# Kernel tuning notes

Measured on AMD Instinct MI355X. Metric: run time of the kernel, lower is better.

The kernel has to match this reference:

```python
import jax, jax.numpy as jnp
import numpy as np

N_CLUSTERS = 128
NUM_ITERS = 10      # fixed Lloyd iterations
LN_EPS = 1e-5       # nn.LayerNorm default eps


def setup_inputs() -> dict:
    key = jax.random.key(0)
    k1, = jax.random.split(key, 1)
    B, N, D = 32, 8192, 64
    patches = jax.random.normal(k1, (B, N, D), dtype=jnp.float32)
    gamma = jnp.ones((D,), dtype=jnp.float32)   # LayerNorm weight
    beta = jnp.zeros((D,), dtype=jnp.float32)   # LayerNorm bias
    return {"patches": patches, "gamma": gamma, "beta": beta}


def _sq_dists(x, x2, c):
    # x: [B,N,D], x2: [B,N,1] (precomputed ||x||^2), c: [B,K,D] -> [B,N,K]
    c2 = jnp.sum(c * c, axis=-1)[:, None, :]                  # [B,1,K]
    return x2 + c2 - 2.0 * jnp.einsum('bnd,bkd->bnk', x, c)


def _kmeans(x):
    B, N, D = x.shape
    K = N_CLUSTERS
    centers0 = x[:, :K, :]                                    # deterministic init: first K points
    x2 = jnp.sum(x * x, axis=-1, keepdims=True)               # [B,N,1]

    def step(c, _):
        d = _sq_dists(x, x2, c)                               # [B,N,K]
        assign = jnp.argmin(d, axis=-1)                       # [B,N]
        oh = jax.nn.one_hot(assign, K, dtype=x.dtype)         # [B,N,K]
        counts = oh.sum(axis=1)                               # [B,K]
        sums = jnp.einsum('bnk,bnd->bkd', oh, x)              # [B,K,D]
        new_c = jnp.where(counts[..., None] > 0,
                          sums / jnp.maximum(counts, 1.0)[..., None],
                          c)                                  # keep empty clusters fixed
        return new_c, None

    centers, _ = jax.lax.scan(step, centers0, None, length=NUM_ITERS)
    dist = _sq_dists(x, x2, centers)                          # [B,N,K]
    soft = jax.nn.softmax(-dist, axis=-1)                     # soft assignment over clusters
    return centers, soft


def reference(patches, gamma, beta):
    # LayerNorm over last dim (biased variance, as in nn.LayerNorm)
    mu = jnp.mean(patches, axis=-1, keepdims=True)
    var = jnp.mean((patches - mu) ** 2, axis=-1, keepdims=True)
    xn = (patches - mu) * jax.lax.rsqrt(var + LN_EPS) * gamma + beta
    centers, soft = _kmeans(xn)
    return centers, soft
```

## Files before the change

### kernel.cpp

```cpp
#include <hip/hip_runtime.h>

#define BATCH 32
#define NPTS  8192
#define DIM   64
#define KC    128
#define NITER 10
#define LN_EPS 1e-5f


__device__ __forceinline__ float dot64(const float4* __restrict__ xv,
                                       const float4* __restrict__ cp) {
    float d0 = 0.f, d1 = 0.f, d2 = 0.f, d3 = 0.f;
#pragma unroll
    for (int j = 0; j < 4; ++j) {
        float4 c0 = cp[4 * j + 0];
        float4 c1 = cp[4 * j + 1];
        float4 c2v = cp[4 * j + 2];
        float4 c3 = cp[4 * j + 3];
        float4 x0 = xv[4 * j + 0];
        float4 x1 = xv[4 * j + 1];
        float4 x2v = xv[4 * j + 2];
        float4 x3 = xv[4 * j + 3];
        d0 = fmaf(x0.w, c0.w, fmaf(x0.z, c0.z, fmaf(x0.y, c0.y, fmaf(x0.x, c0.x, d0))));
        d1 = fmaf(x1.w, c1.w, fmaf(x1.z, c1.z, fmaf(x1.y, c1.y, fmaf(x1.x, c1.x, d1))));
        d2 = fmaf(x2v.w, c2v.w, fmaf(x2v.z, c2v.z, fmaf(x2v.y, c2v.y, fmaf(x2v.x, c2v.x, d2))));
        d3 = fmaf(x3.w, c3.w, fmaf(x3.z, c3.z, fmaf(x3.y, c3.y, fmaf(x3.x, c3.x, d3))));
    }
    return (d0 + d1) + (d2 + d3);
}

__device__ __forceinline__ float sq64(const float4* __restrict__ xv) {
    float a0 = 0.f, a1 = 0.f, a2 = 0.f, a3 = 0.f;
#pragma unroll
    for (int j = 0; j < 16; ++j) {
        float4 t = xv[j];
        a0 = fmaf(t.x, t.x, a0);
        a1 = fmaf(t.y, t.y, a1);
        a2 = fmaf(t.z, t.z, a2);
        a3 = fmaf(t.w, t.w, a3);
    }
    return (a0 + a1) + (a2 + a3);
}

__global__ __launch_bounds__(256) void ln_kernel(const float* __restrict__ patches,
                                                 const float* __restrict__ gamma,
                                                 const float* __restrict__ beta,
                                                 float* __restrict__ xn,
                                                 float* __restrict__ cen,
                                                 float* __restrict__ c2) {
    int row = blockIdx.x * 4 + (threadIdx.x >> 6);
    int lane = threadIdx.x & 63;
    size_t base = (size_t)row * DIM + lane;
    float x = patches[base];

    float s = x;
#pragma unroll
    for (int m = 32; m >= 1; m >>= 1) s += __shfl_xor(s, m, 64);
    float mu = s * (1.0f / 64.0f);
    float dx = x - mu;

    float v = dx * dx;
#pragma unroll
    for (int m = 32; m >= 1; m >>= 1) v += __shfl_xor(v, m, 64);
    float var = v * (1.0f / 64.0f);

    float val = dx * (1.0f / sqrtf(var + LN_EPS)) * gamma[lane] + beta[lane];
    xn[base] = val;

    int n = row & (NPTS - 1);
    int b = row >> 13;
    if (n < KC) {
        cen[((size_t)(b * KC + n)) * DIM + lane] = val;
        float q = val * val;
#pragma unroll
        for (int m = 32; m >= 1; m >>= 1) q += __shfl_xor(q, m, 64);
        if (lane == 0) c2[b * KC + n] = q;
    }
}

__global__ __launch_bounds__(512) void assign_kernel(const float* __restrict__ xn,
                                                     const float* __restrict__ cen,
                                                     const float* __restrict__ c2,
                                                     double* __restrict__ part,
                                                     float* __restrict__ cntpart) {
    __shared__ double ls[KC * 65];
    __shared__ float lc[KC];
    for (int i = threadIdx.x; i < KC * 65; i += 512) ls[i] = 0.0;
    if (threadIdx.x < KC) lc[threadIdx.x] = 0.f;
    __syncthreads();

    int blk = blockIdx.x;
    int b = blk >> 4;
    int p = b * NPTS + ((blk & 15) << 9) + threadIdx.x;

    const float4* xp = (const float4*)(xn + (size_t)p * DIM);
    float4 xv[16];
#pragma unroll
    for (int j = 0; j < 16; ++j) xv[j] = xp[j];
    float x2 = sq64(xv);

    const float4* cp = (const float4*)(cen + (size_t)b * KC * DIM);
    const float* c2p = c2 + b * KC;

    float best = 3.4e38f;
    int bi = 0;
#pragma unroll 2
    for (int k = 0; k < KC; ++k) {
        float dot = dot64(xv, cp + k * 16);
        float t = x2 + c2p[k];
        float d = t - 2.0f * dot;
        if (d < best) { best = d; bi = k; }
    }

    double* dst = ls + bi * 65;
#pragma unroll
    for (int j = 0; j < 16; ++j) {
        atomicAdd(dst + 4 * j + 0, (double)xv[j].x);
        atomicAdd(dst + 4 * j + 1, (double)xv[j].y);
        atomicAdd(dst + 4 * j + 2, (double)xv[j].z);
        atomicAdd(dst + 4 * j + 3, (double)xv[j].w);
    }
    atomicAdd(&lc[bi], 1.0f);
    __syncthreads();

    double* gp = part + (size_t)blk * KC * DIM;
    for (int i = threadIdx.x; i < KC * DIM; i += 512) {
        int k = i >> 6, d = i & 63;
        gp[i] = ls[k * 65 + d];
    }
    if (threadIdx.x < KC) cntpart[blk * KC + threadIdx.x] = lc[threadIdx.x];
}

__global__ __launch_bounds__(256) void update_kernel(const double* __restrict__ part,
                                                     const float* __restrict__ cntpart,
                                                     float* __restrict__ cen,
                                                     float* __restrict__ c2) {
    int row = blockIdx.x * 4 + (threadIdx.x >> 6);
    int lane = threadIdx.x & 63;
    int b = row >> 7;
    int k = row & (KC - 1);

    double s = 0.0;
    float cnt = 0.f;
#pragma unroll
    for (int sub = 0; sub < 16; ++sub) {
        s += part[((size_t)(b * 16 + sub)) * KC * DIM + (size_t)k * DIM + lane];
        cnt += cntpart[(b * 16 + sub) * KC + k];
    }

    size_t idx = (size_t)row * DIM + lane;
    float old = cen[idx];
    float nc = (cnt > 0.f) ? ((float)s / cnt) : old;
    cen[idx] = nc;

    float q = nc * nc;
#pragma unroll
    for (int m = 32; m >= 1; m >>= 1) q += __shfl_xor(q, m, 64);
    if (lane == 0) c2[row] = q;
}

__global__ __launch_bounds__(512) void final_kernel(const float* __restrict__ xn,
                                                    const float* __restrict__ cen,
                                                    const float* __restrict__ c2,
                                                    float* __restrict__ soft) {
    int b = blockIdx.x >> 4;
    int p = b * NPTS + ((blockIdx.x & 15) << 9) + threadIdx.x;

    const float4* xp = (const float4*)(xn + (size_t)p * DIM);
    float4 xv[16];
#pragma unroll
    for (int j = 0; j < 16; ++j) xv[j] = xp[j];
    float x2 = sq64(xv);

    const float4* cp = (const float4*)(cen + (size_t)b * KC * DIM);
    const float* c2p = c2 + b * KC;

    float m = -3.4e38f;
    float ssum = 0.f;
#pragma unroll 2
    for (int k = 0; k < KC; ++k) {
        float dot = dot64(xv, cp + k * 16);
        float t = x2 + c2p[k];
        float z = -(t - 2.0f * dot);
        if (z > m) {
            ssum = ssum * __expf(m - z) + 1.0f;
            m = z;
        } else {
            ssum += __expf(z - m);
        }
    }
    float rinv = 1.0f / ssum;

    float* op = soft + (size_t)p * KC;
#pragma unroll 2
    for (int k = 0; k < KC; ++k) {
        float dot = dot64(xv, cp + k * 16);
        float t = x2 + c2p[k];
        float z = -(t - 2.0f * dot);
        op[k] = __expf(z - m) * rinv;
    }
}

extern "C" void kernel_launch(void* const* d_in, const int* in_sizes, int n_in,
                              void* d_out, int out_size, void* d_ws, size_t ws_size,
                              hipStream_t stream) {
    (void)in_sizes; (void)n_in; (void)out_size; (void)ws_size;
    const float* patches = (const float*)d_in[0];
    const float* gamma = (const float*)d_in[1];
    const float* beta = (const float*)d_in[2];
    float* out = (float*)d_out;

    float* ws = (float*)d_ws;
    float* xn = ws;
    float* cen = xn + (size_t)BATCH * NPTS * DIM;
    float* c2 = cen + (size_t)BATCH * KC * DIM;

    float* soft = out + (size_t)BATCH * KC * DIM;
    double* part = (double*)soft;
    float* cntpart = (float*)(part + (size_t)512 * KC * DIM);

    ln_kernel<<<BATCH * NPTS / 4, 256, 0, stream>>>(patches, gamma, beta, xn, cen, c2);

    for (int it = 0; it < NITER; ++it) {
        assign_kernel<<<BATCH * 16, 512, 0, stream>>>(xn, cen, c2, part, cntpart);
        update_kernel<<<BATCH * KC / 4, 256, 0, stream>>>(part, cntpart, cen, c2);
    }

    hipMemcpyAsync(out, cen, (size_t)BATCH * KC * DIM * sizeof(float),
                   hipMemcpyDeviceToDevice, stream);
    final_kernel<<<BATCH * 16, 512, 0, stream>>>(xn, cen, c2, soft);
}
```

Measured before the change: 1.900 ms.

## Use float LDS atomics, explicit register unrolling, vector soft stores, drop center copy

```diff
diff --git a/kernel.cpp b/kernel.cpp
--- a/kernel.cpp
+++ b/kernel.cpp
@@ -8,39 +8,36 @@
 #define LN_EPS 1e-5f
 
 
-__device__ __forceinline__ float dot64(const float4* __restrict__ xv,
-                                       const float4* __restrict__ cp) {
-    float d0 = 0.f, d1 = 0.f, d2 = 0.f, d3 = 0.f;
-#pragma unroll
-    for (int j = 0; j < 4; ++j) {
-        float4 c0 = cp[4 * j + 0];
-        float4 c1 = cp[4 * j + 1];
-        float4 c2v = cp[4 * j + 2];
-        float4 c3 = cp[4 * j + 3];
-        float4 x0 = xv[4 * j + 0];
-        float4 x1 = xv[4 * j + 1];
-        float4 x2v = xv[4 * j + 2];
-        float4 x3 = xv[4 * j + 3];
-        d0 = fmaf(x0.w, c0.w, fmaf(x0.z, c0.z, fmaf(x0.y, c0.y, fmaf(x0.x, c0.x, d0))));
-        d1 = fmaf(x1.w, c1.w, fmaf(x1.z, c1.z, fmaf(x1.y, c1.y, fmaf(x1.x, c1.x, d1))));
-        d2 = fmaf(x2v.w, c2v.w, fmaf(x2v.z, c2v.z, fmaf(x2v.y, c2v.y, fmaf(x2v.x, c2v.x, d2))));
-        d3 = fmaf(x3.w, c3.w, fmaf(x3.z, c3.z, fmaf(x3.y, c3.y, fmaf(x3.x, c3.x, d3))));
-    }
-    return (d0 + d1) + (d2 + d3);
-}
-
-__device__ __forceinline__ float sq64(const float4* __restrict__ xv) {
-    float a0 = 0.f, a1 = 0.f, a2 = 0.f, a3 = 0.f;
-#pragma unroll
-    for (int j = 0; j < 16; ++j) {
-        float4 t = xv[j];
-        a0 = fmaf(t.x, t.x, a0);
-        a1 = fmaf(t.y, t.y, a1);
-        a2 = fmaf(t.z, t.z, a2);
-        a3 = fmaf(t.w, t.w, a3);
-    }
-    return (a0 + a1) + (a2 + a3);
-}
+#define FMA4(acc, xv, cv) \
+    acc = fmaf((xv).w, (cv).w, fmaf((xv).z, (cv).z, fmaf((xv).y, (cv).y, fmaf((xv).x, (cv).x, (acc)))))
+
+#define DOT16(res, cbase) do {                                            \
+    const float4* _c = (cbase);                                           \
+    float _d0 = 0.f, _d1 = 0.f, _d2 = 0.f, _d3 = 0.f;                     \
+    FMA4(_d0, x0, _c[0]);   FMA4(_d1, x1, _c[1]);                         \
+    FMA4(_d2, x2, _c[2]);   FMA4(_d3, x3, _c[3]);                         \
+    FMA4(_d0, x4, _c[4]);   FMA4(_d1, x5, _c[5]);                         \
+    FMA4(_d2, x6, _c[6]);   FMA4(_d3, x7, _c[7]);                         \
+    FMA4(_d0, x8, _c[8]);   FMA4(_d1, x9, _c[9]);                         \
+    FMA4(_d2, x10, _c[10]); FMA4(_d3, x11, _c[11]);                       \
+    FMA4(_d0, x12, _c[12]); FMA4(_d1, x13, _c[13]);                       \
+    FMA4(_d2, x14, _c[14]); FMA4(_d3, x15, _c[15]);                       \
+    res = (_d0 + _d1) + (_d2 + _d3);                                      \
+} while (0)
+
+#define SQ4(xv) do {                       \
+    a0 = fmaf((xv).x, (xv).x, a0);         \
+    a1 = fmaf((xv).y, (xv).y, a1);         \
+    a2 = fmaf((xv).z, (xv).z, a2);         \
+    a3 = fmaf((xv).w, (xv).w, a3);         \
+} while (0)
+
+#define LOAD_X16(ptr)                                              \
+    const float4* xp = (const float4*)(ptr);                       \
+    float4 x0 = xp[0], x1 = xp[1], x2 = xp[2], x3 = xp[3];         \
+    float4 x4 = xp[4], x5 = xp[5], x6 = xp[6], x7 = xp[7];         \
+    float4 x8 = xp[8], x9 = xp[9], x10 = xp[10], x11 = xp[11];     \
+    float4 x12 = xp[12], x13 = xp[13], x14 = xp[14], x15 = xp[15]
 
 __global__ __launch_bounds__(256) void ln_kernel(const float* __restrict__ patches,
                                                  const float* __restrict__ gamma,
@@ -78,14 +75,14 @@
     }
 }
 
-__global__ __launch_bounds__(512) void assign_kernel(const float* __restrict__ xn,
-                                                     const float* __restrict__ cen,
-                                                     const float* __restrict__ c2,
-                                                     double* __restrict__ part,
-                                                     float* __restrict__ cntpart) {
-    __shared__ double ls[KC * 65];
+__global__ __launch_bounds__(512, 4) void assign_kernel(const float* __restrict__ xn,
+                                                        const float* __restrict__ cen,
+                                                        const float* __restrict__ c2,
+                                                        float* __restrict__ part,
+                                                        float* __restrict__ cntpart) {
+    __shared__ float ls[KC * 65];
     __shared__ float lc[KC];
-    for (int i = threadIdx.x; i < KC * 65; i += 512) ls[i] = 0.0;
+    for (int i = threadIdx.x; i < KC * 65; i += 512) ls[i] = 0.f;
     if (threadIdx.x < KC) lc[threadIdx.x] = 0.f;
     __syncthreads();
 
@@ -93,37 +90,40 @@
     int b = blk >> 4;
     int p = b * NPTS + ((blk & 15) << 9) + threadIdx.x;
 
-    const float4* xp = (const float4*)(xn + (size_t)p * DIM);
-    float4 xv[16];
-#pragma unroll
-    for (int j = 0; j < 16; ++j) xv[j] = xp[j];
-    float x2 = sq64(xv);
+    LOAD_X16(xn + (size_t)p * DIM);
+    float a0 = 0.f, a1 = 0.f, a2 = 0.f, a3 = 0.f;
+    SQ4(x0); SQ4(x1); SQ4(x2); SQ4(x3); SQ4(x4); SQ4(x5); SQ4(x6); SQ4(x7);
+    SQ4(x8); SQ4(x9); SQ4(x10); SQ4(x11); SQ4(x12); SQ4(x13); SQ4(x14); SQ4(x15);
+    float xsq = (a0 + a1) + (a2 + a3);
 
     const float4* cp = (const float4*)(cen + (size_t)b * KC * DIM);
     const float* c2p = c2 + b * KC;
 
     float best = 3.4e38f;
     int bi = 0;
-#pragma unroll 2
     for (int k = 0; k < KC; ++k) {
-        float dot = dot64(xv, cp + k * 16);
-        float t = x2 + c2p[k];
+        float dot;
+        DOT16(dot, cp + k * 16);
+        float t = xsq + c2p[k];
         float d = t - 2.0f * dot;
         if (d < best) { best = d; bi = k; }
     }
 
-    double* dst = ls + bi * 65;
-#pragma unroll
-    for (int j = 0; j < 16; ++j) {
-        atomicAdd(dst + 4 * j + 0, (double)xv[j].x);
-        atomicAdd(dst + 4 * j + 1, (double)xv[j].y);
-        atomicAdd(dst + 4 * j + 2, (double)xv[j].z);
-        atomicAdd(dst + 4 * j + 3, (double)xv[j].w);
-    }
+    float* dst = ls + bi * 65;
+#define ATM4(j, xv)                            \
+    atomicAdd(dst + 4 * (j) + 0, (xv).x);      \
+    atomicAdd(dst + 4 * (j) + 1, (xv).y);      \
+    atomicAdd(dst + 4 * (j) + 2, (xv).z);      \
+    atomicAdd(dst + 4 * (j) + 3, (xv).w)
+    ATM4(0, x0); ATM4(1, x1); ATM4(2, x2); ATM4(3, x3);
+    ATM4(4, x4); ATM4(5, x5); ATM4(6, x6); ATM4(7, x7);
+    ATM4(8, x8); ATM4(9, x9); ATM4(10, x10); ATM4(11, x11);
+    ATM4(12, x12); ATM4(13, x13); ATM4(14, x14); ATM4(15, x15);
+#undef ATM4
     atomicAdd(&lc[bi], 1.0f);
     __syncthreads();
 
-    double* gp = part + (size_t)blk * KC * DIM;
+    float* gp = part + (size_t)blk * KC * DIM;
     for (int i = threadIdx.x; i < KC * DIM; i += 512) {
         int k = i >> 6, d = i & 63;
         gp[i] = ls[k * 65 + d];
@@ -131,7 +131,7 @@
     if (threadIdx.x < KC) cntpart[blk * KC + threadIdx.x] = lc[threadIdx.x];
 }
 
-__global__ __launch_bounds__(256) void update_kernel(const double* __restrict__ part,
+__global__ __launch_bounds__(256) void update_kernel(const float* __restrict__ part,
                                                      const float* __restrict__ cntpart,
                                                      float* __restrict__ cen,
                                                      float* __restrict__ c2) {
@@ -144,7 +144,7 @@
     float cnt = 0.f;
 #pragma unroll
     for (int sub = 0; sub < 16; ++sub) {
-        s += part[((size_t)(b * 16 + sub)) * KC * DIM + (size_t)k * DIM + lane];
+        s += (double)part[((size_t)(b * 16 + sub)) * KC * DIM + (size_t)k * DIM + lane];
         cnt += cntpart[(b * 16 + sub) * KC + k];
     }
 
@@ -159,28 +159,28 @@
     if (lane == 0) c2[row] = q;
 }
 
-__global__ __launch_bounds__(512) void final_kernel(const float* __restrict__ xn,
-                                                    const float* __restrict__ cen,
-                                                    const float* __restrict__ c2,
-                                                    float* __restrict__ soft) {
+__global__ __launch_bounds__(512, 4) void final_kernel(const float* __restrict__ xn,
+                                                       const float* __restrict__ cen,
+                                                       const float* __restrict__ c2,
+                                                       float* __restrict__ soft) {
     int b = blockIdx.x >> 4;
     int p = b * NPTS + ((blockIdx.x & 15) << 9) + threadIdx.x;
 
-    const float4* xp = (const float4*)(xn + (size_t)p * DIM);
-    float4 xv[16];
-#pragma unroll
-    for (int j = 0; j < 16; ++j) xv[j] = xp[j];
-    float x2 = sq64(xv);
+    LOAD_X16(xn + (size_t)p * DIM);
+    float a0 = 0.f, a1 = 0.f, a2 = 0.f, a3 = 0.f;
+    SQ4(x0); SQ4(x1); SQ4(x2); SQ4(x3); SQ4(x4); SQ4(x5); SQ4(x6); SQ4(x7);
+    SQ4(x8); SQ4(x9); SQ4(x10); SQ4(x11); SQ4(x12); SQ4(x13); SQ4(x14); SQ4(x15);
+    float xsq = (a0 + a1) + (a2 + a3);
 
     const float4* cp = (const float4*)(cen + (size_t)b * KC * DIM);
     const float* c2p = c2 + b * KC;
 
     float m = -3.4e38f;
     float ssum = 0.f;
-#pragma unroll 2
     for (int k = 0; k < KC; ++k) {
-        float dot = dot64(xv, cp + k * 16);
-        float t = x2 + c2p[k];
+        float dot;
+        DOT16(dot, cp + k * 16);
+        float t = xsq + c2p[k];
         float z = -(t - 2.0f * dot);
         if (z > m) {
             ssum = ssum * __expf(m - z) + 1.0f;
@@ -191,13 +191,19 @@
     }
     float rinv = 1.0f / ssum;
 
-    float* op = soft + (size_t)p * KC;
-#pragma unroll 2
-    for (int k = 0; k < KC; ++k) {
-        float dot = dot64(xv, cp + k * 16);
-        float t = x2 + c2p[k];
-        float z = -(t - 2.0f * dot);
-        op[k] = __expf(z - m) * rinv;
+    float4* op = (float4*)(soft + (size_t)p * KC);
+    for (int kb = 0; kb < KC / 4; ++kb) {
+        float e[4];
+#pragma unroll
+        for (int u = 0; u < 4; ++u) {
+            int k = kb * 4 + u;
+            float dot;
+            DOT16(dot, cp + k * 16);
+            float t = xsq + c2p[k];
+            float z = -(t - 2.0f * dot);
+            e[u] = __expf(z - m) * rinv;
+        }
+        op[kb] = make_float4(e[0], e[1], e[2], e[3]);
     }
 }
 
@@ -212,12 +218,12 @@
 
     float* ws = (float*)d_ws;
     float* xn = ws;
-    float* cen = xn + (size_t)BATCH * NPTS * DIM;
-    float* c2 = cen + (size_t)BATCH * KC * DIM;
-
+    float* c2 = xn + (size_t)BATCH * NPTS * DIM;
+
+    float* cen = out;
     float* soft = out + (size_t)BATCH * KC * DIM;
-    double* part = (double*)soft;
-    float* cntpart = (float*)(part + (size_t)512 * KC * DIM);
+    float* part = soft;
+    float* cntpart = part + (size_t)512 * KC * DIM;
 
     ln_kernel<<<BATCH * NPTS / 4, 256, 0, stream>>>(patches, gamma, beta, xn, cen, c2);
 
@@ -226,7 +232,5 @@
         update_kernel<<<BATCH * KC / 4, 256, 0, stream>>>(part, cntpart, cen, c2);
     }
 
-    hipMemcpyAsync(out, cen, (size_t)BATCH * KC * DIM * sizeof(float),
-                   hipMemcpyDeviceToDevice, stream);
     final_kernel<<<BATCH * 16, 512, 0, stream>>>(xn, cen, c2, soft);
 }
```

Result: slower. 2.192 ms (+15.4%).
